# Kernel tuning notes

Hardware: AMD Instinct MI355X
Metric: run time of the kernel (lower is better)

Reference implementation:

```python
import jax, jax.numpy as jnp
import numpy as np

NS, L, H = 8, 2048, 1024
M, E, K = 4096, 8, 2
EPS = 1e-9

def setup_inputs() -> dict:
    key = jax.random.key(0)
    ks = jax.random.split(key, 5)
    s = 0.02
    return {
        "x": jax.random.normal(ks[0], (NS, L, H), jnp.float32),
        "Wr": jax.random.normal(ks[1], (H, E), jnp.float32) * s,
        "br": jnp.zeros((E,), jnp.float32),
        "W1": jax.random.normal(ks[2], (E, H, M), jnp.float32) * s,
        "b1": jnp.zeros((E, M), jnp.float32),
        "W2": jax.random.normal(ks[3], (E, M, H), jnp.float32) * s,
        "b2": jnp.zeros((E, H), jnp.float32),
    }

def reference(x, Wr, br, W1, b1, W2, b2):
    ns, seq, h = x.shape
    flat = x.reshape(-1, h)                      # (N, H); grouping only reshapes, math is per-token
    logits = flat @ Wr + br                      # (N, E)
    probs = jax.nn.softmax(logits, axis=-1)
    vals, idx = jax.lax.top_k(probs, K)          # (N, K)
    w = vals / (jnp.sum(vals, axis=-1, keepdims=True) + EPS)
    out_acc = jnp.zeros_like(flat)
    weight_acc = jnp.zeros((flat.shape[0],), flat.dtype)
    for e in range(E):                           # fixed small expert loop
        we = jnp.sum(w * (idx == e), axis=-1)    # (N,) combine weight for expert e
        hmid = jax.nn.gelu(flat @ W1[e] + b1[e], approximate=False)
        y = hmid @ W2[e] + b2[e]
        out_acc = out_acc + we[:, None] * y
        weight_acc = weight_acc + we
    out = out_acc / (weight_acc[:, None] + EPS)
    return out.reshape(ns, seq, h)
```

## Files before the change

kernel.cpp:

```cpp
#include <hip/hip_runtime.h>
#include <hip/hip_bf16.h>
#include <math.h>

#define NTOK 16384
#define HDIM 1024
#define MDIM 4096
#define NEXP 8
#define EPSV 1e-9f
#define RTOK 32

typedef unsigned short u16;
typedef __attribute__((ext_vector_type(4))) float f32x4;
typedef __attribute__((ext_vector_type(8))) __bf16 bf16x8;
typedef __attribute__((ext_vector_type(8))) unsigned short u16x8;
typedef __attribute__((ext_vector_type(4))) unsigned short u16x4;

#define ASYNC_COPY16(gptr, lptr) \
    __builtin_amdgcn_global_load_lds( \
        (const __attribute__((address_space(1))) void*)(gptr), \
        (__attribute__((address_space(3))) void*)(lptr), 16, 0, 0)

static __device__ __forceinline__ u16 f2bf(float f) {
    unsigned int u = __builtin_bit_cast(unsigned int, f);
    u += 0x7fff + ((u >> 16) & 1);
    return (u16)(u >> 16);
}

static __device__ __forceinline__ float gelu_f(float v) {
    float z2 = -1.5957691216f * v * (1.f + 0.044715f * v * v);
    return v / (1.f + __expf(z2));
}

__global__ __launch_bounds__(256) void router_kernel(
    const float* __restrict__ x, const float* __restrict__ Wr,
    const float* __restrict__ br,
    int* __restrict__ counts, int* __restrict__ ltok, float* __restrict__ lcf,
    u16* __restrict__ xb)
{
    __shared__ int   lcount[NEXP];
    __shared__ int   lbase[NEXP];
    __shared__ int   ltokL[NEXP][RTOK];
    __shared__ float lcfL[NEXP][RTOK];

    int t = threadIdx.x;
    if (t < NEXP) lcount[t] = 0;
    __syncthreads();

    int wave = t >> 6, lane = t & 63;

    for (int it = 0; it < RTOK / 4; ++it) {
        int tok = blockIdx.x * RTOK + it * 4 + wave;
        const float* xr = x + (size_t)tok * HDIM + lane * 16;

        f32x4 xv[4];
        #pragma unroll
        for (int q = 0; q < 4; q++) xv[q] = *reinterpret_cast<const f32x4*>(xr + q * 4);

        u16x8 ob0, ob1;
        #pragma unroll
        for (int j = 0; j < 4; j++) {
            ob0[j]     = f2bf(xv[0][j]);
            ob0[4 + j] = f2bf(xv[1][j]);
            ob1[j]     = f2bf(xv[2][j]);
            ob1[4 + j] = f2bf(xv[3][j]);
        }
        u16* xo = xb + (size_t)tok * HDIM + lane * 16;
        *reinterpret_cast<u16x8*>(xo)     = ob0;
        *reinterpret_cast<u16x8*>(xo + 8) = ob1;

        f32x4 acc0 = {0.f, 0.f, 0.f, 0.f};
        f32x4 acc1 = {0.f, 0.f, 0.f, 0.f};
        #pragma unroll
        for (int q = 0; q < 4; q++) {
            #pragma unroll
            for (int j = 0; j < 4; j++) {
                int h = lane * 16 + q * 4 + j;
                const float* wrow = Wr + (size_t)h * NEXP;
                f32x4 w0 = *reinterpret_cast<const f32x4*>(wrow);
                f32x4 w1 = *reinterpret_cast<const f32x4*>(wrow + 4);
                acc0 += xv[q][j] * w0;
                acc1 += xv[q][j] * w1;
            }
        }
        float a[NEXP];
        #pragma unroll
        for (int e = 0; e < 4; e++) { a[e] = acc0[e]; a[4 + e] = acc1[e]; }
        #pragma unroll
        for (int e = 0; e < NEXP; e++) {
            #pragma unroll
            for (int s = 1; s < 64; s <<= 1) a[e] += __shfl_xor(a[e], s, 64);
        }
        if (lane == 0) {
            float l[NEXP], m = -1e30f;
            #pragma unroll
            for (int e = 0; e < NEXP; e++) { l[e] = a[e] + br[e]; m = fmaxf(m, l[e]); }
            float p[NEXP], s = 0.f;
            #pragma unroll
            for (int e = 0; e < NEXP; e++) { p[e] = expf(l[e] - m); s += p[e]; }
            int i0 = 0; float v0 = p[0];
            #pragma unroll
            for (int e = 1; e < NEXP; e++) if (p[e] > v0) { v0 = p[e]; i0 = e; }
            int i1 = -1; float v1 = -1.f;
            #pragma unroll
            for (int e = 0; e < NEXP; e++) if (e != i0 && p[e] > v1) { v1 = p[e]; i1 = e; }
            v0 /= s; v1 /= s;
            float sw = v0 + v1;
            float w0 = v0 / (sw + EPSV), w1 = v1 / (sw + EPSV);
            float wa = w0 + w1;
            float c0 = w0 / (wa + EPSV), c1 = w1 / (wa + EPSV);
            int q0 = atomicAdd(&lcount[i0], 1);
            ltokL[i0][q0] = tok; lcfL[i0][q0] = c0;
            int q1 = atomicAdd(&lcount[i1], 1);
            ltokL[i1][q1] = tok; lcfL[i1][q1] = c1;
        }
    }
    __syncthreads();
    if (t < NEXP) lbase[t] = atomicAdd(&counts[t], lcount[t]);
    __syncthreads();
    #pragma unroll
    for (int e = 0; e < NEXP; e++) {
        int n = lcount[e], b = lbase[e];
        for (int j = t; j < n; j += 256) {
            ltok[e * NTOK + b + j] = ltokL[e][j];
            lcf[e * NTOK + b + j]  = lcfL[e][j];
        }
    }
}

__global__ void bases_kernel(const int* __restrict__ counts, int* __restrict__ bases)
{
    if (threadIdx.x == 0) {
        int acc = 0;
        #pragma unroll
        for (int e = 0; e < NEXP; e++) { bases[e] = acc; acc += counts[e]; }
    }
}

__global__ __launch_bounds__(256) void transpose_cvt_kernel(
    const float* __restrict__ in, u16* __restrict__ out, int R, int C)
{
    __shared__ float tile[32][33];
    const float* ine = in + (size_t)blockIdx.z * R * C;
    u16* oute = out + (size_t)blockIdx.z * R * C;
    int r0 = blockIdx.y * 32, c0 = blockIdx.x * 32;
    int t = threadIdx.x;
    int r = t >> 3, cq = t & 7;
    f32x4 v = *reinterpret_cast<const f32x4*>(ine + (size_t)(r0 + r) * C + c0 + cq * 4);
    #pragma unroll
    for (int j = 0; j < 4; j++) tile[r][cq * 4 + j] = v[j];
    __syncthreads();
    int c = t >> 3, rq = t & 7;
    u16x4 o;
    #pragma unroll
    for (int j = 0; j < 4; j++) o[j] = f2bf(tile[rq * 4 + j][c]);
    *reinterpret_cast<u16x4*>(oute + (size_t)(c0 + c) * R + r0 + rq * 4) = o;
}

template<int EPI, int GX, int GY>
__global__ __launch_bounds__(512) void gemm_kernel(
    const u16* __restrict__ A,
    const u16* __restrict__ BT_all,
    const float* __restrict__ bias_all,
    const int* __restrict__ counts,
    const int* __restrict__ bases,
    const int* __restrict__ ltok,
    const float* __restrict__ lcf,
    u16* __restrict__ hmid,
    float* __restrict__ out,
    int K, int P, int Astride, int eStart)
{
    int gz = gridDim.z;
    int nwg = GX * GY * gz;
    int orig = blockIdx.x + GX * (blockIdx.y + GY * blockIdx.z);
    int qq = nwg >> 3, rr = nwg & 7;
    int xcd = orig & 7, sub = orig >> 3;
    int wgid = (xcd < rr ? xcd * (qq + 1) : rr * (qq + 1) + (xcd - rr) * qq) + sub;
    int bx = wgid & (GX - 1);
    int rem = wgid / GX;
    int by = rem & (GY - 1);
    int bz = rem / GY;

    int e = eStart + bz;
    int nrows = counts[e];
    int row0 = by * 256;
    if (row0 >= nrows) return;
    int p0 = bx * 128;
    int slotbase = bases[e];
    const u16*   BT   = BT_all + (size_t)e * P * K;
    const float* bias = bias_all + (size_t)e * P;
    const int*   lte  = ltok + (size_t)e * NTOK;
    const float* lcfe = lcf  + (size_t)e * NTOK;

    __shared__ u16 As[256][64];
    __shared__ u16 Bs[128][64];

    int t = threadIdx.x;
    int wv = t >> 6, lane = t & 63;
    int lrow8 = lane >> 3;
    int lcol8 = lane & 7;
    int schunk = lcol8 ^ lrow8;

    const u16* aptr[4];
    const u16* bptr[2];
    #pragma unroll
    for (int i = 0; i < 4; i++) {
        int pos  = row0 + wv * 32 + i * 8 + lrow8;
        int posc = min(pos, nrows - 1);
        int arow = (EPI == 0) ? lte[posc] : (slotbase + posc);
        aptr[i] = A + (size_t)arow * Astride + schunk * 8;
    }
    #pragma unroll
    for (int j = 0; j < 2; j++) {
        int prow = p0 + wv * 16 + j * 8 + lrow8;
        bptr[j] = BT + (size_t)prow * K + schunk * 8;
    }

    int wr = (wv >> 1) * 64, wc = (wv & 1) * 64;
    int lr = lane & 15, lg = lane >> 4;
    int lr7 = lr & 7;

    f32x4 acc[4][4];
    #pragma unroll
    for (int m = 0; m < 4; m++)
        #pragma unroll
        for (int nn = 0; nn < 4; nn++) acc[m][nn] = (f32x4){0.f, 0.f, 0.f, 0.f};

    for (int k0 = 0; k0 < K; k0 += 64) {
        #pragma unroll
        for (int i = 0; i < 4; i++)
            ASYNC_COPY16(aptr[i] + k0, &As[wv * 32 + i * 8][0]);
        #pragma unroll
        for (int j = 0; j < 2; j++)
            ASYNC_COPY16(bptr[j] + k0, &Bs[wv * 16 + j * 8][0]);
        __syncthreads();
        #pragma unroll
        for (int kk = 0; kk < 64; kk += 32) {
            int q = kk >> 3;
            bf16x8 af[4], bf[4];
            #pragma unroll
            for (int m = 0; m < 4; m++)
                af[m] = *reinterpret_cast<const bf16x8*>(
                    &As[wr + m * 16 + lr][((q + lg) ^ lr7) * 8]);
            #pragma unroll
            for (int nn = 0; nn < 4; nn++)
                bf[nn] = *reinterpret_cast<const bf16x8*>(
                    &Bs[wc + nn * 16 + lr][((q + lg) ^ lr7) * 8]);
            #pragma unroll
            for (int m = 0; m < 4; m++)
                #pragma unroll
                for (int nn = 0; nn < 4; nn++)
                    acc[m][nn] = __builtin_amdgcn_mfma_f32_16x16x32_bf16(
                        af[m], bf[nn], acc[m][nn], 0, 0, 0);
        }
        __syncthreads();
    }

    if (EPI == 0) {
        #pragma unroll
        for (int m = 0; m < 4; m++) {
            #pragma unroll
            for (int r2 = 0; r2 < 4; r2++) {
                int pos = row0 + wr + m * 16 + lg * 4 + r2;
                if (pos < nrows) {
                    size_t ho = (size_t)(slotbase + pos) * MDIM;
                    #pragma unroll
                    for (int nn = 0; nn < 4; nn++) {
                        int col = p0 + wc + nn * 16 + lr;
                        float v = acc[m][nn][r2] + bias[col];
                        hmid[ho + col] = f2bf(gelu_f(v));
                    }
                }
            }
        }
    } else {
        #pragma unroll
        for (int m = 0; m < 4; m++) {
            #pragma unroll
            for (int r2 = 0; r2 < 4; r2++) {
                int pos = row0 + wr + m * 16 + lg * 4 + r2;
                if (pos < nrows) {
                    int tokr = lte[pos];
                    float cf = lcfe[pos];
                    float* orow = out + (size_t)tokr * HDIM;
                    #pragma unroll
                    for (int nn = 0; nn < 4; nn++) {
                        int col = p0 + wc + nn * 16 + lr;
                        float v = (acc[m][nn][r2] + bias[col]) * cf;
                        atomicAdd(orow + col, v);
                    }
                }
            }
        }
    }
}

extern "C" void kernel_launch(void* const* d_in, const int* in_sizes, int n_in,
                              void* d_out, int out_size, void* d_ws, size_t ws_size,
                              hipStream_t stream)
{
    const float* x  = (const float*)d_in[0];
    const float* Wr = (const float*)d_in[1];
    const float* br = (const float*)d_in[2];
    const float* W1 = (const float*)d_in[3];
    const float* b1 = (const float*)d_in[4];
    const float* W2 = (const float*)d_in[5];
    const float* b2 = (const float*)d_in[6];
    float* out = (float*)d_out;

    char* ws = (char*)d_ws;
    size_t off = 0;
    auto alloc = [&](size_t bytes) {
        void* p = ws + off;
        off = (off + bytes + 255) & ~(size_t)255;
        return p;
    };
    int*   counts = (int*)  alloc(NEXP * 4);
    int*   bases  = (int*)  alloc(NEXP * 4);
    int*   ltok   = (int*)  alloc((size_t)NEXP * NTOK * 4);
    float* lcf    = (float*)alloc((size_t)NEXP * NTOK * 4);
    u16*   xb     = (u16*)  alloc((size_t)NTOK * HDIM * 2);
    u16*   w1t    = (u16*)  alloc((size_t)NEXP * MDIM * HDIM * 2);
    u16*   w2t    = (u16*)  alloc((size_t)NEXP * HDIM * MDIM * 2);
    size_t fixed_end = off;
    bool grouped = (ws_size >= fixed_end + (size_t)2 * NTOK * MDIM * 2);
    u16* hmid = (u16*)alloc((grouped ? (size_t)2 * NTOK : (size_t)NTOK) * MDIM * 2);

    hipMemsetAsync(counts, 0, NEXP * 4, stream);
    hipMemsetAsync(d_out, 0, (size_t)out_size * sizeof(float), stream);

    transpose_cvt_kernel<<<dim3(MDIM / 32, HDIM / 32, NEXP), 256, 0, stream>>>(W1, w1t, HDIM, MDIM);
    transpose_cvt_kernel<<<dim3(HDIM / 32, MDIM / 32, NEXP), 256, 0, stream>>>(W2, w2t, MDIM, HDIM);
    router_kernel<<<NTOK / RTOK, 256, 0, stream>>>(x, Wr, br, counts, ltok, lcf, xb);

    if (grouped) {
        bases_kernel<<<1, 64, 0, stream>>>(counts, bases);
        gemm_kernel<0, MDIM / 128, NTOK / 256>
            <<<dim3(MDIM / 128, NTOK / 256, NEXP), 512, 0, stream>>>(
            xb, w1t, b1, counts, bases, ltok, lcf, hmid, nullptr,
            HDIM, MDIM, HDIM, 0);
        gemm_kernel<1, HDIM / 128, NTOK / 256>
            <<<dim3(HDIM / 128, NTOK / 256, NEXP), 512, 0, stream>>>(
            hmid, w2t, b2, counts, bases, ltok, lcf, nullptr, out,
            MDIM, HDIM, MDIM, 0);
    } else {
        hipMemsetAsync(bases, 0, NEXP * 4, stream);
        for (int e = 0; e < NEXP; e++) {
            gemm_kernel<0, MDIM / 128, NTOK / 256>
                <<<dim3(MDIM / 128, NTOK / 256, 1), 512, 0, stream>>>(
                xb, w1t, b1, counts, bases, ltok, lcf, hmid, nullptr,
                HDIM, MDIM, HDIM, e);
            gemm_kernel<1, HDIM / 128, NTOK / 256>
                <<<dim3(HDIM / 128, NTOK / 256, 1), 512, 0, stream>>>(
                hmid, w2t, b2, counts, bases, ltok, lcf, nullptr, out,
                MDIM, HDIM, MDIM, e);
        }
    }
}
```

Measured before the change: 961.4 us.

## Overlap next K-tile loads with MFMA, reorder down-proj tiles, merge transposes

The GEMM main loop now loads all LDS fragments for a K-tile into registers, passes a barrier, and issues the async global-to-LDS copies for the next tile before running the MFMAs. Global load latency then overlaps with compute on a single LDS buffer. The second GEMM uses a row-fast workgroup ordering so consecutive workgroups share the same weight columns and hmid rows differ, aiming at better L2 reuse. The two weight transpose-convert launches are merged into one. Holding two halves of the fragments raises register pressure.

```diff
diff --git a/kernel.cpp b/kernel.cpp
--- a/kernel.cpp
+++ b/kernel.cpp
@@ -137,12 +137,28 @@
 }
 
 __global__ __launch_bounds__(256) void transpose_cvt_kernel(
-    const float* __restrict__ in, u16* __restrict__ out, int R, int C)
+    const float* __restrict__ W1, const float* __restrict__ W2,
+    u16* __restrict__ w1t, u16* __restrict__ w2t)
 {
     __shared__ float tile[32][33];
-    const float* ine = in + (size_t)blockIdx.z * R * C;
-    u16* oute = out + (size_t)blockIdx.z * R * C;
-    int r0 = blockIdx.y * 32, c0 = blockIdx.x * 32;
+    int z = blockIdx.z;
+    int R, C;
+    const float* ine;
+    u16* oute;
+    if (z < NEXP) {
+        R = HDIM; C = MDIM;
+        ine  = W1 + (size_t)z * R * C;
+        oute = w1t + (size_t)z * R * C;
+    } else {
+        R = MDIM; C = HDIM;
+        ine  = W2 + (size_t)(z - NEXP) * R * C;
+        oute = w2t + (size_t)(z - NEXP) * R * C;
+    }
+    int tiles_x = C >> 5;
+    int ti = blockIdx.x;
+    int c0 = (ti & (tiles_x - 1)) * 32;
+    int r0 = (ti / tiles_x) * 32;
+
     int t = threadIdx.x;
     int r = t >> 3, cq = t & 7;
     f32x4 v = *reinterpret_cast<const f32x4*>(ine + (size_t)(r0 + r) * C + c0 + cq * 4);
@@ -156,7 +172,7 @@
     *reinterpret_cast<u16x4*>(oute + (size_t)(c0 + c) * R + r0 + rq * 4) = o;
 }
 
-template<int EPI, int GX, int GY>
+template<int EPI, int YFAST, int GX, int GY>
 __global__ __launch_bounds__(512) void gemm_kernel(
     const u16* __restrict__ A,
     const u16* __restrict__ BT_all,
@@ -175,10 +191,18 @@
     int qq = nwg >> 3, rr = nwg & 7;
     int xcd = orig & 7, sub = orig >> 3;
     int wgid = (xcd < rr ? xcd * (qq + 1) : rr * (qq + 1) + (xcd - rr) * qq) + sub;
-    int bx = wgid & (GX - 1);
-    int rem = wgid / GX;
-    int by = rem & (GY - 1);
-    int bz = rem / GY;
+    int bx, by, bz;
+    if (YFAST) {
+        by = wgid & (GY - 1);
+        int rem = wgid / GY;
+        bx = rem & (GX - 1);
+        bz = rem / GX;
+    } else {
+        bx = wgid & (GX - 1);
+        int rem = wgid / GX;
+        by = rem & (GY - 1);
+        bz = rem / GY;
+    }
 
     int e = eStart + bz;
     int nrows = counts[e];
@@ -225,34 +249,46 @@
         #pragma unroll
         for (int nn = 0; nn < 4; nn++) acc[m][nn] = (f32x4){0.f, 0.f, 0.f, 0.f};
 
-    for (int k0 = 0; k0 < K; k0 += 64) {
+    auto stage = [&](int k0) {
         #pragma unroll
         for (int i = 0; i < 4; i++)
             ASYNC_COPY16(aptr[i] + k0, &As[wv * 32 + i * 8][0]);
         #pragma unroll
         for (int j = 0; j < 2; j++)
             ASYNC_COPY16(bptr[j] + k0, &Bs[wv * 16 + j * 8][0]);
-        __syncthreads();
-        #pragma unroll
-        for (int kk = 0; kk < 64; kk += 32) {
-            int q = kk >> 3;
-            bf16x8 af[4], bf[4];
+    };
+
+    stage(0);
+    for (int k0 = 0; k0 < K; k0 += 64) {
+        asm volatile("s_waitcnt vmcnt(0)" ::: "memory");
+        __builtin_amdgcn_s_barrier();
+
+        bf16x8 af[2][4], bf[2][4];
+        #pragma unroll
+        for (int h = 0; h < 2; h++) {
+            int q = h * 4;
             #pragma unroll
             for (int m = 0; m < 4; m++)
-                af[m] = *reinterpret_cast<const bf16x8*>(
+                af[h][m] = *reinterpret_cast<const bf16x8*>(
                     &As[wr + m * 16 + lr][((q + lg) ^ lr7) * 8]);
             #pragma unroll
             for (int nn = 0; nn < 4; nn++)
-                bf[nn] = *reinterpret_cast<const bf16x8*>(
+                bf[h][nn] = *reinterpret_cast<const bf16x8*>(
                     &Bs[wc + nn * 16 + lr][((q + lg) ^ lr7) * 8]);
+        }
+        asm volatile("s_waitcnt lgkmcnt(0)" ::: "memory");
+        __builtin_amdgcn_s_barrier();
+
+        if (k0 + 64 < K) stage(k0 + 64);
+
+        #pragma unroll
+        for (int h = 0; h < 2; h++)
             #pragma unroll
             for (int m = 0; m < 4; m++)
                 #pragma unroll
                 for (int nn = 0; nn < 4; nn++)
                     acc[m][nn] = __builtin_amdgcn_mfma_f32_16x16x32_bf16(
-                        af[m], bf[nn], acc[m][nn], 0, 0, 0);
-        }
-        __syncthreads();
+                        af[h][m], bf[h][nn], acc[m][nn], 0, 0, 0);
     }
 
     if (EPI == 0) {
@@ -328,28 +364,28 @@
     hipMemsetAsync(counts, 0, NEXP * 4, stream);
     hipMemsetAsync(d_out, 0, (size_t)out_size * sizeof(float), stream);
 
-    transpose_cvt_kernel<<<dim3(MDIM / 32, HDIM / 32, NEXP), 256, 0, stream>>>(W1, w1t, HDIM, MDIM);
-    transpose_cvt_kernel<<<dim3(HDIM / 32, MDIM / 32, NEXP), 256, 0, stream>>>(W2, w2t, MDIM, HDIM);
+    transpose_cvt_kernel<<<dim3((HDIM * MDIM) / 1024, 1, 2 * NEXP), 256, 0, stream>>>(
+        W1, W2, w1t, w2t);
     router_kernel<<<NTOK / RTOK, 256, 0, stream>>>(x, Wr, br, counts, ltok, lcf, xb);
 
     if (grouped) {
         bases_kernel<<<1, 64, 0, stream>>>(counts, bases);
-        gemm_kernel<0, MDIM / 128, NTOK / 256>
+        gemm_kernel<0, 0, MDIM / 128, NTOK / 256>
             <<<dim3(MDIM / 128, NTOK / 256, NEXP), 512, 0, stream>>>(
             xb, w1t, b1, counts, bases, ltok, lcf, hmid, nullptr,
             HDIM, MDIM, HDIM, 0);
-        gemm_kernel<1, HDIM / 128, NTOK / 256>
+        gemm_kernel<1, 1, HDIM / 128, NTOK / 256>
             <<<dim3(HDIM / 128, NTOK / 256, NEXP), 512, 0, stream>>>(
             hmid, w2t, b2, counts, bases, ltok, lcf, nullptr, out,
             MDIM, HDIM, MDIM, 0);
     } else {
         hipMemsetAsync(bases, 0, NEXP * 4, stream);
         for (int e = 0; e < NEXP; e++) {
-            gemm_kernel<0, MDIM / 128, NTOK / 256>
+            gemm_kernel<0, 0, MDIM / 128, NTOK / 256>
                 <<<dim3(MDIM / 128, NTOK / 256, 1), 512, 0, stream>>>(
                 xb, w1t, b1, counts, bases, ltok, lcf, hmid, nullptr,
                 HDIM, MDIM, HDIM, e);
-            gemm_kernel<1, HDIM / 128, NTOK / 256>
+            gemm_kernel<1, 1, HDIM / 128, NTOK / 256>
                 <<<dim3(HDIM / 128, NTOK / 256, 1), 512, 0, stream>>>(
                 hmid, w2t, b2, counts, bases, ltok, lcf, nullptr, out,
                 MDIM, HDIM, MDIM, e);
```

Measured after the change: 1.218 ms. 26.7% more time.
